# Kernel optimization log

Measured on AMD Instinct MI355X. Metric: run time of the kernel, lower is better.

The kernel has to match this reference:

```python
import jax, jax.numpy as jnp
import numpy as np

H, HK, D, WIN = 16, 4, 128, 1024  # n_head, n_kv_head, head_dim, left window


def rmsnorm(x):
    eps = jnp.asarray(jnp.finfo(x.dtype).eps, x.dtype)
    return x * jax.lax.rsqrt(jnp.mean(x * x, axis=-1, keepdims=True) + eps)


def rope(x, cos, sin):
    d = x.shape[-1] // 2
    x1, x2 = x[..., :d], x[..., d:]
    return jnp.concatenate([x1 * cos + x2 * sin, x1 * -sin + x2 * cos], axis=-1)


def setup_inputs() -> dict:
    key = jax.random.key(0)
    ks = jax.random.split(key, 12)
    B, T, C = 4, 2048, 2048
    t = jnp.arange(T, dtype=jnp.float32)[:, None]
    inv = 1.0 / (10000.0 ** (jnp.arange(D // 2, dtype=jnp.float32) / (D // 2)))
    ang = t * inv[None, :]  # [T, D/2]
    return {
        "x": jax.random.normal(ks[0], (B, T, C), jnp.float32),
        "x0": jax.random.normal(ks[1], (B, T, C), jnp.float32),
        "ve": jnp.zeros((B, T, C), jnp.float32),  # unused in add_init_qkv branch
        "cos": jnp.cos(ang)[None, :, None, :],  # [1,T,1,D/2]
        "sin": jnp.sin(ang)[None, :, None, :],
        "Wq": jax.random.normal(ks[2], (H * D, C), jnp.float32) * 0.02,
        "Wk": jax.random.normal(ks[3], (HK * D, C), jnp.float32) * 0.02,
        "Wv": jax.random.normal(ks[4], (HK * D, C), jnp.float32) * 0.02,
        "Wproj": jax.random.normal(ks[5], (C, H * D), jnp.float32) * 0.02,
        "alpha_q": jnp.ones((1,), jnp.float32),
        "beta_q": jax.random.uniform(ks[6], (1,), jnp.float32),
        "alpha_k": jnp.ones((1,), jnp.float32),
        "beta_k": jax.random.uniform(ks[7], (1,), jnp.float32),
        "alpha_v": jnp.ones((1,), jnp.float32),
        "beta_v": jax.random.uniform(ks[8], (1,), jnp.float32),
    }


def reference(x, x0, ve, cos, sin, Wq, Wk, Wv, Wproj,
              alpha_q, beta_q, alpha_k, beta_k, alpha_v, beta_v):
    B, T, C = x.shape
    g = H // HK  # GQA group size

    q = (x @ Wq.T).reshape(B, T, H, D)
    k = (x @ Wk.T).reshape(B, T, HK, D)
    v = (x @ Wv.T).reshape(B, T, HK, D)
    v_init = v

    # is_target + add_init_qkv + learn_init_coeffs: blend with projections of norm(x0)
    x0n = rmsnorm(x0)
    cqx = (x0n @ Wq.T).reshape(B, T, H, D)
    ckx = (x0n @ Wk.T).reshape(B, T, HK, D)
    cvx = (x0n @ Wv.T).reshape(B, T, HK, D)
    q = alpha_q * q + beta_q * cqx
    k = alpha_k * k + beta_k * ckx
    v = alpha_v * v + beta_v * cvx

    # rotary + qk-norm + 1.2 scale
    q = rmsnorm(rope(q, cos, sin)) * 1.2
    k = rmsnorm(rope(k, cos, sin)) * 1.2

    qg = q.reshape(B, T, HK, g, D)
    scale = 1.0 / np.sqrt(D)
    scores = jnp.einsum('bqhgd,bkhd->bhgqk', qg, k) * scale  # [B,HK,g,T,T]
    i = jnp.arange(T)[:, None]
    j = jnp.arange(T)[None, :]
    mask = (j <= i) & (i - j <= WIN)
    scores = jnp.where(mask, scores, -jnp.inf)
    p = jax.nn.softmax(scores, axis=-1)
    y = jnp.einsum('bhgqk,bkhd->bqhgd', p, v).reshape(B, T, H * D)

    y = y @ Wproj.T
    return (y, v_init)
```

## Files before the change

kernel.cpp:

```cpp
#include <hip/hip_runtime.h>
#include <hip/hip_bf16.h>
#include <math.h>


using bf16 = __hip_bfloat16;
typedef __attribute__((ext_vector_type(8))) short bf16x8;
typedef __attribute__((ext_vector_type(4))) short bf16x4;
typedef __attribute__((ext_vector_type(4))) float f32x4;

constexpr int Bb = 4, Ts = 2048, Cc = 2048, NH = 16, NKV = 4, Dh = 128, WIN = 1024;
constexpr float EPS = 1.1920929e-07f;

__device__ __forceinline__ void gld16(void* lds, const void* g) {
  __builtin_amdgcn_global_load_lds(
      (__attribute__((address_space(1))) unsigned int*)((void*)g),
      (__attribute__((address_space(3))) unsigned int*)lds, 16, 0, 0);
}

__device__ __forceinline__ unsigned short bfbits(float f) {
  bf16 h = __float2bfloat16(f);
  return __builtin_bit_cast(unsigned short, h);
}

__device__ __forceinline__ void store_out(float* p, float v) { *p = v; }
__device__ __forceinline__ void store_out(bf16* p, float v) { *p = __float2bfloat16(v); }

__device__ __forceinline__ f32x4 mfma16(bf16x4 a, bf16x4 b, f32x4 c) {
#if __has_builtin(__builtin_amdgcn_mfma_f32_16x16x16bf16_1k)
  return __builtin_amdgcn_mfma_f32_16x16x16bf16_1k(a, b, c, 0, 0, 0);
#else
  bf16x8 a8 = {a[0], a[1], a[2], a[3], 0, 0, 0, 0};
  bf16x8 b8 = {b[0], b[1], b[2], b[3], 0, 0, 0, 0};
  return __builtin_amdgcn_mfma_f32_16x16x32_bf16(a8, b8, c, 0, 0, 0);
#endif
}

__global__ __launch_bounds__(256) void convert_w(const float* __restrict__ src,
                                                 bf16* __restrict__ dst, int n4) {
  int i = blockIdx.x * 256 + threadIdx.x;
  if (i < n4) {
    float4 v = ((const float4*)src)[i];
    ushort4 u;
    u.x = bfbits(v.x); u.y = bfbits(v.y); u.z = bfbits(v.z); u.w = bfbits(v.w);
    ((ushort4*)dst)[i] = u;
  }
}

__global__ __launch_bounds__(256) void prep(
    const float* __restrict__ x, const float* __restrict__ x0,
    const float* aq_p, const float* bq_p, const float* ak_p, const float* bk_p,
    bf16* __restrict__ xq, bf16* __restrict__ xk,
    bf16* __restrict__ xb, bf16* __restrict__ x0n) {
  const int row = blockIdx.x, tid = threadIdx.x;
  const float4* xr = (const float4*)(x + (size_t)row * Cc);
  const float4* nr = (const float4*)(x0 + (size_t)row * Cc);
  float4 xa[2], na[2];
  float ss = 0.f;
#pragma unroll
  for (int j = 0; j < 2; ++j) {
    xa[j] = xr[tid + j * 256];
    na[j] = nr[tid + j * 256];
    ss += na[j].x * na[j].x + na[j].y * na[j].y + na[j].z * na[j].z + na[j].w * na[j].w;
  }
#pragma unroll
  for (int o = 32; o; o >>= 1) ss += __shfl_xor(ss, o);
  __shared__ float red[4];
  if ((tid & 63) == 0) red[tid >> 6] = ss;
  __syncthreads();
  const float rms = rsqrtf((red[0] + red[1] + red[2] + red[3]) * (1.f / Cc) + EPS);
  const float aq = *aq_p, bq = *bq_p, ak = *ak_p, bk = *bk_p;
#pragma unroll
  for (int j = 0; j < 2; ++j) {
    const size_t base = (size_t)row * Cc + (size_t)(tid + j * 256) * 4;
    float nx[4] = {na[j].x * rms, na[j].y * rms, na[j].z * rms, na[j].w * rms};
    float xv[4] = {xa[j].x, xa[j].y, xa[j].z, xa[j].w};
    ushort4 uq, uk, ub, un;
    uq.x = bfbits(aq * xv[0] + bq * nx[0]); uq.y = bfbits(aq * xv[1] + bq * nx[1]);
    uq.z = bfbits(aq * xv[2] + bq * nx[2]); uq.w = bfbits(aq * xv[3] + bq * nx[3]);
    uk.x = bfbits(ak * xv[0] + bk * nx[0]); uk.y = bfbits(ak * xv[1] + bk * nx[1]);
    uk.z = bfbits(ak * xv[2] + bk * nx[2]); uk.w = bfbits(ak * xv[3] + bk * nx[3]);
    ub.x = bfbits(xv[0]); ub.y = bfbits(xv[1]); ub.z = bfbits(xv[2]); ub.w = bfbits(xv[3]);
    un.x = bfbits(nx[0]); un.y = bfbits(nx[1]); un.z = bfbits(nx[2]); un.w = bfbits(nx[3]);
    *(ushort4*)(xq + base) = uq;
    *(ushort4*)(xk + base) = uk;
    *(ushort4*)(xb + base) = ub;
    *(ushort4*)(x0n + base) = un;
  }
}

template <typename OutT>
__device__ __forceinline__ void gemm_body(
    const bf16* __restrict__ A, const bf16* __restrict__ W,
    OutT* __restrict__ C, int N, int K) {
  __shared__ unsigned short sA[128 * 64];
  __shared__ unsigned short sB[128 * 64];
  const int tid = threadIdx.x, wave = tid >> 6, lane = tid & 63;
  const int quad = lane >> 4, l15 = lane & 15;
  const int bm = blockIdx.x * 128, bn = blockIdx.y * 128;
  const int wm = (wave >> 1) * 64, wn = (wave & 1) * 64;
  const int srow = wave * 32 + (lane >> 3);
  const int scol = (lane & 7) * 8;

  f32x4 acc[4][4] = {};

  for (int k0 = 0; k0 < K; k0 += 64) {
#pragma unroll
    for (int i = 0; i < 4; ++i) {
      gld16(&sA[(wave * 32 + i * 8) * 64], &A[(size_t)(bm + srow + i * 8) * K + k0 + scol]);
      gld16(&sB[(wave * 32 + i * 8) * 64], &W[(size_t)(bn + srow + i * 8) * K + k0 + scol]);
    }
    __syncthreads();
#pragma unroll
    for (int kk = 0; kk < 2; ++kk) {
      bf16x8 af[4], bfr[4];
#pragma unroll
      for (int t = 0; t < 4; ++t)
        af[t] = *(const bf16x8*)&sA[(wm + t * 16 + l15) * 64 + kk * 32 + quad * 8];
#pragma unroll
      for (int t = 0; t < 4; ++t)
        bfr[t] = *(const bf16x8*)&sB[(wn + t * 16 + l15) * 64 + kk * 32 + quad * 8];
#pragma unroll
      for (int tm = 0; tm < 4; ++tm)
#pragma unroll
        for (int tn = 0; tn < 4; ++tn)
          acc[tm][tn] = __builtin_amdgcn_mfma_f32_16x16x32_bf16(af[tm], bfr[tn], acc[tm][tn], 0, 0, 0);
    }
    __syncthreads();
  }
#pragma unroll
  for (int tm = 0; tm < 4; ++tm)
#pragma unroll
    for (int tn = 0; tn < 4; ++tn)
#pragma unroll
      for (int r = 0; r < 4; ++r) {
        const int row = bm + wm + tm * 16 + quad * 4 + r;
        const int col = bn + wn + tn * 16 + l15;
        store_out(&C[(size_t)row * N + col], acc[tm][tn][r]);
      }
}

template <typename OutT>
__global__ __launch_bounds__(256) void gemm_bt(
    const bf16* __restrict__ A, const bf16* __restrict__ W,
    OutT* __restrict__ C, int N, int K) {
  gemm_body<OutT>(A, W, C, N, K);
}

struct GemmTriple { const bf16* A; const bf16* W; bf16* C; };
struct GemmTriple3 { GemmTriple t[3]; };

__global__ __launch_bounds__(256) void gemm_bt3(GemmTriple3 g, int N, int K) {
  const GemmTriple tr = g.t[blockIdx.z];
  gemm_body<bf16>(tr.A, tr.W, tr.C, N, K);
}

__global__ __launch_bounds__(256) void post_qk(
    const bf16* __restrict__ pre, const float* __restrict__ cosp,
    const float* __restrict__ sinp, bf16* __restrict__ outh, int nh, float mult) {
  const int wid = blockIdx.x * 4 + (threadIdx.x >> 6);
  const int lane = threadIdx.x & 63;
  const int h = wid % nh;
  const int bt = wid / nh;
  const int t = bt & (Ts - 1);
  const int b = bt >> 11;
  const size_t src = (size_t)bt * (size_t)(nh * Dh) + (size_t)h * Dh;
  float x1 = __bfloat162float(pre[src + lane]);
  float x2 = __bfloat162float(pre[src + 64 + lane]);
  float c = cosp[t * 64 + lane], s = sinp[t * 64 + lane];
  float o1 = x1 * c + x2 * s;
  float o2 = x2 * c - x1 * s;
  float ss = o1 * o1 + o2 * o2;
#pragma unroll
  for (int o = 32; o; o >>= 1) ss += __shfl_xor(ss, o);
  const float r = rsqrtf(ss * (1.f / Dh) + EPS) * mult;
  const size_t dst = ((size_t)(b * nh + h) * Ts + t) * Dh;
  outh[dst + lane] = __float2bfloat16(o1 * r);
  outh[dst + 64 + lane] = __float2bfloat16(o2 * r);
}

__global__ __launch_bounds__(256) void post_v(
    const bf16* __restrict__ vinit, const bf16* __restrict__ cvx,
    const float* av_p, const float* bv_p,
    bf16* __restrict__ vth, float* __restrict__ vout) {
  __shared__ unsigned short vt[128 * 65];
  const int t0 = blockIdx.x * 64;
  const int b = blockIdx.y >> 2, hk = blockIdx.y & 3;
  const float av = *av_p, bv = *bv_p;
  const int tid = threadIdx.x;
  for (int j = 0; j < 32; ++j) {
    const int e = j * 256 + tid;
    const int tl = e >> 7, d = e & 127;
    const size_t src = (size_t)(b * Ts + t0 + tl) * (NKV * Dh) + hk * Dh + d;
    const float vi = __bfloat162float(vinit[src]);
    const float cv = __bfloat162float(cvx[src]);
    vout[src] = vi;
    vt[d * 65 + tl] = bfbits(av * vi + bv * cv);
  }
  __syncthreads();
#pragma unroll
  for (int j = 0; j < 4; ++j) {
    const int g = j * 256 + tid;
    const int d = g >> 3, t8 = (g & 7) * 8;
    const unsigned short* p = &vt[d * 65 + t8];
    uint4 u;
    u.x = p[0] | ((unsigned int)p[1] << 16);
    u.y = p[2] | ((unsigned int)p[3] << 16);
    u.z = p[4] | ((unsigned int)p[5] << 16);
    u.w = p[6] | ((unsigned int)p[7] << 16);
    *(uint4*)&vth[((size_t)(b * NKV + hk) * Dh + d) * Ts + t0 + t8] = u;
  }
}

__global__ __launch_bounds__(256) void attn(
    const bf16* __restrict__ qh, const bf16* __restrict__ kh,
    const bf16* __restrict__ vth, bf16* __restrict__ att) {
  __shared__ unsigned short sK[64 * 128];
  __shared__ unsigned short sV[128 * 64];

  const int tid = threadIdx.x, wave = tid >> 6, lane = tid & 63;
  const int quad = lane >> 4, l15 = lane & 15;
  const int q0 = blockIdx.x * 128;
  const int b = blockIdx.y >> 4, h = blockIdx.y & 15, hk = h >> 2;

  const bf16* Qp = qh + (size_t)(b * NH + h) * Ts * Dh;
  const bf16* Kp = kh + (size_t)(b * NKV + hk) * Ts * Dh;
  const bf16* Vp = vth + (size_t)(b * NKV + hk) * Dh * Ts;

  const int qw = q0 + wave * 32;

  bf16x8 qf[2][4];
#pragma unroll
  for (int tm = 0; tm < 2; ++tm)
#pragma unroll
    for (int kk = 0; kk < 4; ++kk)
      qf[tm][kk] = *(const bf16x8*)&Qp[(size_t)(qw + tm * 16 + l15) * Dh + kk * 32 + quad * 8];

  f32x4 of[2][8] = {};
  float m_i[2] = {-__builtin_inff(), -__builtin_inff()};
  float l_i[2] = {0.f, 0.f};

  const int krow = lane >> 4, kgp = lane & 15;
  const int vrow = lane >> 3, vgp = lane & 7;

  const int jt_lo = q0 >= WIN ? (q0 - WIN) >> 6 : 0;
  const int jt_hi = (q0 + 127) >> 6;

  for (int jt = jt_lo; jt <= jt_hi; ++jt) {
    const int j0 = jt << 6;
    __syncthreads();
#pragma unroll
    for (int i = 0; i < 4; ++i) {
      const int row = wave * 16 + i * 4 + krow;
      gld16(&sK[(wave * 16 + i * 4) * 128],
            &Kp[(size_t)(j0 + row) * Dh + (kgp ^ (row & 15)) * 8]);
      const int d = wave * 32 + i * 8 + vrow;
      gld16(&sV[(wave * 32 + i * 8) * 64],
            &Vp[(size_t)d * Ts + j0 + (vgp ^ (d & 7)) * 8]);
    }
    __syncthreads();

    if (j0 > qw + 31 || qw > j0 + 63 + WIN) continue;

    f32x4 sfT[4][2];
#pragma unroll
    for (int tn = 0; tn < 4; ++tn) {
      bf16x8 kf[4];
#pragma unroll
      for (int kk = 0; kk < 4; ++kk)
        kf[kk] = *(const bf16x8*)&sK[(tn * 16 + l15) * 128 + (((kk * 4 + quad) ^ l15) * 8)];
#pragma unroll
      for (int tm = 0; tm < 2; ++tm) {
        f32x4 a = {};
#pragma unroll
        for (int kk = 0; kk < 4; ++kk)
          a = __builtin_amdgcn_mfma_f32_16x16x32_bf16(kf[kk], qf[tm][kk], a, 0, 0, 0);
        sfT[tn][tm] = a;
      }
    }

    float alpha[2];
    bf16x4 pf[2][4];
#pragma unroll
    for (int tm = 0; tm < 2; ++tm) {
      const int dq = (qw + tm * 16 + l15) - (j0 + quad * 4);
      float mloc = -__builtin_inff();
#pragma unroll
      for (int tn = 0; tn < 4; ++tn)
#pragma unroll
        for (int r = 0; r < 4; ++r) {
          const unsigned diff = (unsigned)(dq - tn * 16 - r);
          float s = (diff <= (unsigned)WIN) ? sfT[tn][tm][r] : -__builtin_inff();
          sfT[tn][tm][r] = s;
          mloc = fmaxf(mloc, s);
        }
      mloc = fmaxf(mloc, __shfl_xor(mloc, 16));
      mloc = fmaxf(mloc, __shfl_xor(mloc, 32));
      const float mnew = fmaxf(m_i[tm], mloc);
      alpha[tm] = __builtin_amdgcn_exp2f(m_i[tm] - mnew);
      m_i[tm] = mnew;
      float rs = 0.f;
#pragma unroll
      for (int tn = 0; tn < 4; ++tn) {
        bf16x4 p4;
#pragma unroll
        for (int r = 0; r < 4; ++r) {
          const float p = __builtin_amdgcn_exp2f(sfT[tn][tm][r] - mnew);
          rs += p;
          p4[r] = (short)bfbits(p);
        }
        pf[tm][tn] = p4;
      }
      rs += __shfl_xor(rs, 16);
      rs += __shfl_xor(rs, 32);
      l_i[tm] = l_i[tm] * alpha[tm] + rs;
    }

#pragma unroll
    for (int tm = 0; tm < 2; ++tm) {
      float ar[4];
#pragma unroll
      for (int r = 0; r < 4; ++r) ar[r] = __shfl(alpha[tm], quad * 4 + r);
#pragma unroll
      for (int dn = 0; dn < 8; ++dn)
#pragma unroll
        for (int r = 0; r < 4; ++r) of[tm][dn][r] *= ar[r];
    }

#pragma unroll
    for (int tn = 0; tn < 4; ++tn) {
      const int gsw = (tn * 2) ^ (l15 & 7);
#pragma unroll
      for (int dn = 0; dn < 8; ++dn) {
        const int d = dn * 16 + l15;
        const bf16x4 vf = *(const bf16x4*)&sV[d * 64 + ((gsw ^ (quad >> 1)) * 8) + (quad & 1) * 4];
        of[0][dn] = mfma16(pf[0][tn], vf, of[0][dn]);
        of[1][dn] = mfma16(pf[1][tn], vf, of[1][dn]);
      }
    }
  }

#pragma unroll
  for (int tm = 0; tm < 2; ++tm) {
#pragma unroll
    for (int r = 0; r < 4; ++r) {
      const float lr = __shfl(l_i[tm], quad * 4 + r);
      const float inv = 1.f / lr;
      const int qr = qw + tm * 16 + quad * 4 + r;
      bf16* dst = att + (size_t)(b * Ts + qr) * (NH * Dh) + h * Dh;
#pragma unroll
      for (int dn = 0; dn < 8; ++dn)
        dst[dn * 16 + l15] = __float2bfloat16(of[tm][dn][r] * inv);
    }
  }
}

extern "C" void kernel_launch(void* const* d_in, const int* in_sizes, int n_in,
                              void* d_out, int out_size, void* d_ws, size_t ws_size,
                              hipStream_t stream) {
  const float* x = (const float*)d_in[0];
  const float* x0 = (const float*)d_in[1];
  const float* cosp = (const float*)d_in[3];
  const float* sinp = (const float*)d_in[4];
  const float* Wq = (const float*)d_in[5];
  const float* Wk = (const float*)d_in[6];
  const float* Wv = (const float*)d_in[7];
  const float* Wp = (const float*)d_in[8];
  const float* aq = (const float*)d_in[9];
  const float* bq = (const float*)d_in[10];
  const float* ak = (const float*)d_in[11];
  const float* bk = (const float*)d_in[12];
  const float* av = (const float*)d_in[13];
  const float* bv = (const float*)d_in[14];

  char* ws = (char*)d_ws;
  const size_t MB = 1024ull * 1024;
  bf16* xq = (bf16*)(ws + 0 * MB);
  bf16* xk = (bf16*)(ws + 32 * MB);
  bf16* xb = (bf16*)(ws + 64 * MB);
  bf16* x0n = (bf16*)(ws + 96 * MB);
  bf16* vinit = (bf16*)(ws + 128 * MB);
  bf16* cvx = (bf16*)(ws + 136 * MB);
  bf16* Wqb = (bf16*)(ws + 144 * MB);
  bf16* Wkb = (bf16*)(ws + 152 * MB);
  bf16* Wvb = (bf16*)(ws + 154 * MB);
  bf16* Wpb = (bf16*)(ws + 156 * MB);
  bf16* att = xq;
  bf16* qh = xk;
  bf16* kh = xb;
  bf16* vth = (bf16*)(ws + 72 * MB);

  float* y = (float*)d_out;
  float* vout = (float*)d_out + (size_t)Bb * Ts * Cc;
  bf16* q_pre = (bf16*)d_out;
  bf16* k_pre = (bf16*)vout;

  convert_w<<<4096, 256, 0, stream>>>(Wq, Wqb, 1048576);
  convert_w<<<1024, 256, 0, stream>>>(Wk, Wkb, 262144);
  convert_w<<<1024, 256, 0, stream>>>(Wv, Wvb, 262144);
  convert_w<<<4096, 256, 0, stream>>>(Wp, Wpb, 1048576);

  prep<<<8192, 256, 0, stream>>>(x, x0, aq, bq, ak, bk, xq, xk, xb, x0n);

  gemm_bt<bf16><<<dim3(64, 16), 256, 0, stream>>>(xq, Wqb, q_pre, 2048, 2048);

  GemmTriple3 g3;
  g3.t[0] = {xk, Wkb, k_pre};
  g3.t[1] = {xb, Wvb, vinit};
  g3.t[2] = {x0n, Wvb, cvx};
  gemm_bt3<<<dim3(64, 4, 3), 256, 0, stream>>>(g3, 512, 2048);

  const float qmult = 1.2f * 0.08838834764831845f * 1.4426950408889634f;
  post_qk<<<32768, 256, 0, stream>>>(q_pre, cosp, sinp, qh, NH, qmult);
  post_qk<<<8192, 256, 0, stream>>>(k_pre, cosp, sinp, kh, NKV, 1.2f);
  post_v<<<dim3(32, 16), 256, 0, stream>>>(vinit, cvx, av, bv, vth, vout);

  attn<<<dim3(16, 64), 256, 0, stream>>>(qh, kh, vth, att);

  gemm_bt<float><<<dim3(64, 16), 256, 0, stream>>>(att, Wpb, y, 2048, 2048);
}
```

Baseline: 790.5 us.

## Merge small launches, pre-blend V input, skip interior masking and rescale

Combines the four weight conversions into one kernel and the Q/K rope-norm passes into one launch. It also blends x and normalized x0 with the V coefficients in prep, so the V GEMM writes blended V directly and v_init is written as fp32 straight to the output, removing the post_v pass. In attention, interior tiles skip mask evaluation and the output rescale is skipped when the running max is unchanged. This trades a few extra branches for fewer launches and less intermediate memory traffic.

```diff
diff --git a/kernel.cpp b/kernel.cpp
--- a/kernel.cpp
+++ b/kernel.cpp
@@ -35,22 +35,30 @@
 #endif
 }
 
-__global__ __launch_bounds__(256) void convert_w(const float* __restrict__ src,
-                                                 bf16* __restrict__ dst, int n4) {
+__global__ __launch_bounds__(256) void convert_all(
+    const float* __restrict__ s0, const float* __restrict__ s1,
+    const float* __restrict__ s2, const float* __restrict__ s3,
+    bf16* __restrict__ d0, bf16* __restrict__ d1,
+    bf16* __restrict__ d2, bf16* __restrict__ d3) {
   int i = blockIdx.x * 256 + threadIdx.x;
-  if (i < n4) {
-    float4 v = ((const float4*)src)[i];
-    ushort4 u;
-    u.x = bfbits(v.x); u.y = bfbits(v.y); u.z = bfbits(v.z); u.w = bfbits(v.w);
-    ((ushort4*)dst)[i] = u;
-  }
+  const float* s;
+  bf16* d;
+  if (i < 1048576) { s = s0; d = d0; }
+  else if (i < 1310720) { s = s1; d = d1; i -= 1048576; }
+  else if (i < 1572864) { s = s2; d = d2; i -= 1310720; }
+  else { s = s3; d = d3; i -= 1572864; }
+  float4 v = ((const float4*)s)[i];
+  ushort4 u;
+  u.x = bfbits(v.x); u.y = bfbits(v.y); u.z = bfbits(v.z); u.w = bfbits(v.w);
+  ((ushort4*)d)[i] = u;
 }
 
 __global__ __launch_bounds__(256) void prep(
     const float* __restrict__ x, const float* __restrict__ x0,
     const float* aq_p, const float* bq_p, const float* ak_p, const float* bk_p,
+    const float* av_p, const float* bv_p,
     bf16* __restrict__ xq, bf16* __restrict__ xk,
-    bf16* __restrict__ xb, bf16* __restrict__ x0n) {
+    bf16* __restrict__ xb, bf16* __restrict__ xvm) {
   const int row = blockIdx.x, tid = threadIdx.x;
   const float4* xr = (const float4*)(x + (size_t)row * Cc);
   const float4* nr = (const float4*)(x0 + (size_t)row * Cc);
@@ -68,23 +76,24 @@
   if ((tid & 63) == 0) red[tid >> 6] = ss;
   __syncthreads();
   const float rms = rsqrtf((red[0] + red[1] + red[2] + red[3]) * (1.f / Cc) + EPS);
-  const float aq = *aq_p, bq = *bq_p, ak = *ak_p, bk = *bk_p;
+  const float aq = *aq_p, bq = *bq_p, ak = *ak_p, bk = *bk_p, av = *av_p, bv = *bv_p;
 #pragma unroll
   for (int j = 0; j < 2; ++j) {
     const size_t base = (size_t)row * Cc + (size_t)(tid + j * 256) * 4;
     float nx[4] = {na[j].x * rms, na[j].y * rms, na[j].z * rms, na[j].w * rms};
     float xv[4] = {xa[j].x, xa[j].y, xa[j].z, xa[j].w};
-    ushort4 uq, uk, ub, un;
+    ushort4 uq, uk, ub, uv;
     uq.x = bfbits(aq * xv[0] + bq * nx[0]); uq.y = bfbits(aq * xv[1] + bq * nx[1]);
     uq.z = bfbits(aq * xv[2] + bq * nx[2]); uq.w = bfbits(aq * xv[3] + bq * nx[3]);
     uk.x = bfbits(ak * xv[0] + bk * nx[0]); uk.y = bfbits(ak * xv[1] + bk * nx[1]);
     uk.z = bfbits(ak * xv[2] + bk * nx[2]); uk.w = bfbits(ak * xv[3] + bk * nx[3]);
     ub.x = bfbits(xv[0]); ub.y = bfbits(xv[1]); ub.z = bfbits(xv[2]); ub.w = bfbits(xv[3]);
-    un.x = bfbits(nx[0]); un.y = bfbits(nx[1]); un.z = bfbits(nx[2]); un.w = bfbits(nx[3]);
+    uv.x = bfbits(av * xv[0] + bv * nx[0]); uv.y = bfbits(av * xv[1] + bv * nx[1]);
+    uv.z = bfbits(av * xv[2] + bv * nx[2]); uv.w = bfbits(av * xv[3] + bv * nx[3]);
     *(ushort4*)(xq + base) = uq;
     *(ushort4*)(xk + base) = uk;
     *(ushort4*)(xb + base) = ub;
-    *(ushort4*)(x0n + base) = un;
+    *(ushort4*)(xvm + base) = uv;
   }
 }
 
@@ -146,21 +155,31 @@
   gemm_body<OutT>(A, W, C, N, K);
 }
 
-struct GemmTriple { const bf16* A; const bf16* W; bf16* C; };
-struct GemmTriple3 { GemmTriple t[3]; };
-
-__global__ __launch_bounds__(256) void gemm_bt3(GemmTriple3 g, int N, int K) {
-  const GemmTriple tr = g.t[blockIdx.z];
-  gemm_body<bf16>(tr.A, tr.W, tr.C, N, K);
-}
-
-__global__ __launch_bounds__(256) void post_qk(
-    const bf16* __restrict__ pre, const float* __restrict__ cosp,
-    const float* __restrict__ sinp, bf16* __restrict__ outh, int nh, float mult) {
+struct GT { const bf16* A; const bf16* W; void* C; int isf32; };
+struct GT3 { GT t[3]; };
+
+__global__ __launch_bounds__(256) void gemm_bt3(GT3 g, int N, int K) {
+  const GT tr = g.t[blockIdx.z];
+  if (tr.isf32)
+    gemm_body<float>(tr.A, tr.W, (float*)tr.C, N, K);
+  else
+    gemm_body<bf16>(tr.A, tr.W, (bf16*)tr.C, N, K);
+}
+
+__global__ __launch_bounds__(256) void post_qk2(
+    const bf16* __restrict__ qpre, const bf16* __restrict__ kpre,
+    const float* __restrict__ cosp, const float* __restrict__ sinp,
+    bf16* __restrict__ qh, bf16* __restrict__ kh, float qmult, float kmult) {
   const int wid = blockIdx.x * 4 + (threadIdx.x >> 6);
   const int lane = threadIdx.x & 63;
-  const int h = wid % nh;
-  const int bt = wid / nh;
+  const bf16* pre;
+  bf16* outh;
+  int nh, idx;
+  float mult;
+  if (wid < Bb * Ts * NH) { pre = qpre; outh = qh; nh = NH; idx = wid; mult = qmult; }
+  else { pre = kpre; outh = kh; nh = NKV; idx = wid - Bb * Ts * NH; mult = kmult; }
+  const int h = idx % nh;
+  const int bt = idx / nh;
   const int t = bt & (Ts - 1);
   const int b = bt >> 11;
   const size_t src = (size_t)bt * (size_t)(nh * Dh) + (size_t)h * Dh;
@@ -178,23 +197,17 @@
   outh[dst + 64 + lane] = __float2bfloat16(o2 * r);
 }
 
-__global__ __launch_bounds__(256) void post_v(
-    const bf16* __restrict__ vinit, const bf16* __restrict__ cvx,
-    const float* av_p, const float* bv_p,
-    bf16* __restrict__ vth, float* __restrict__ vout) {
+__global__ __launch_bounds__(256) void transpose_v(
+    const unsigned short* __restrict__ vtmp, bf16* __restrict__ vth) {
   __shared__ unsigned short vt[128 * 65];
   const int t0 = blockIdx.x * 64;
   const int b = blockIdx.y >> 2, hk = blockIdx.y & 3;
-  const float av = *av_p, bv = *bv_p;
   const int tid = threadIdx.x;
+#pragma unroll
   for (int j = 0; j < 32; ++j) {
     const int e = j * 256 + tid;
     const int tl = e >> 7, d = e & 127;
-    const size_t src = (size_t)(b * Ts + t0 + tl) * (NKV * Dh) + hk * Dh + d;
-    const float vi = __bfloat162float(vinit[src]);
-    const float cv = __bfloat162float(cvx[src]);
-    vout[src] = vi;
-    vt[d * 65 + tl] = bfbits(av * vi + bv * cv);
+    vt[d * 65 + tl] = vtmp[(size_t)(b * Ts + t0 + tl) * (NKV * Dh) + hk * Dh + d];
   }
   __syncthreads();
 #pragma unroll
@@ -278,33 +291,47 @@
       }
     }
 
+    const bool interior = (j0 + 63 <= qw) && (qw + 31 - j0 <= WIN);
+
     float alpha[2];
+    bool upd[2];
     bf16x4 pf[2][4];
 #pragma unroll
     for (int tm = 0; tm < 2; ++tm) {
-      const int dq = (qw + tm * 16 + l15) - (j0 + quad * 4);
       float mloc = -__builtin_inff();
-#pragma unroll
-      for (int tn = 0; tn < 4; ++tn)
-#pragma unroll
-        for (int r = 0; r < 4; ++r) {
-          const unsigned diff = (unsigned)(dq - tn * 16 - r);
-          float s = (diff <= (unsigned)WIN) ? sfT[tn][tm][r] : -__builtin_inff();
-          sfT[tn][tm][r] = s;
-          mloc = fmaxf(mloc, s);
-        }
+      if (interior) {
+#pragma unroll
+        for (int tn = 0; tn < 4; ++tn)
+#pragma unroll
+          for (int r = 0; r < 4; ++r) mloc = fmaxf(mloc, sfT[tn][tm][r]);
+      } else {
+        const int dq = (qw + tm * 16 + l15) - (j0 + quad * 4);
+#pragma unroll
+        for (int tn = 0; tn < 4; ++tn)
+#pragma unroll
+          for (int r = 0; r < 4; ++r) {
+            const unsigned diff = (unsigned)(dq - tn * 16 - r);
+            float s = (diff <= (unsigned)WIN) ? sfT[tn][tm][r] : -__builtin_inff();
+            sfT[tn][tm][r] = s;
+            mloc = fmaxf(mloc, s);
+          }
+      }
       mloc = fmaxf(mloc, __shfl_xor(mloc, 16));
       mloc = fmaxf(mloc, __shfl_xor(mloc, 32));
-      const float mnew = fmaxf(m_i[tm], mloc);
-      alpha[tm] = __builtin_amdgcn_exp2f(m_i[tm] - mnew);
-      m_i[tm] = mnew;
+      upd[tm] = __any(mloc > m_i[tm]);
+      alpha[tm] = 1.f;
+      if (upd[tm]) {
+        const float mnew = fmaxf(m_i[tm], mloc);
+        alpha[tm] = __builtin_amdgcn_exp2f(m_i[tm] - mnew);
+        m_i[tm] = mnew;
+      }
       float rs = 0.f;
 #pragma unroll
       for (int tn = 0; tn < 4; ++tn) {
         bf16x4 p4;
 #pragma unroll
         for (int r = 0; r < 4; ++r) {
-          const float p = __builtin_amdgcn_exp2f(sfT[tn][tm][r] - mnew);
+          const float p = __builtin_amdgcn_exp2f(sfT[tn][tm][r] - m_i[tm]);
           rs += p;
           p4[r] = (short)bfbits(p);
         }
@@ -317,13 +344,15 @@
 
 #pragma unroll
     for (int tm = 0; tm < 2; ++tm) {
-      float ar[4];
-#pragma unroll
-      for (int r = 0; r < 4; ++r) ar[r] = __shfl(alpha[tm], quad * 4 + r);
-#pragma unroll
-      for (int dn = 0; dn < 8; ++dn)
-#pragma unroll
-        for (int r = 0; r < 4; ++r) of[tm][dn][r] *= ar[r];
+      if (upd[tm]) {
+        float ar[4];
+#pragma unroll
+        for (int r = 0; r < 4; ++r) ar[r] = __shfl(alpha[tm], quad * 4 + r);
+#pragma unroll
+        for (int dn = 0; dn < 8; ++dn)
+#pragma unroll
+          for (int r = 0; r < 4; ++r) of[tm][dn][r] *= ar[r];
+      }
     }
 
 #pragma unroll
@@ -377,9 +406,9 @@
   bf16* xq = (bf16*)(ws + 0 * MB);
   bf16* xk = (bf16*)(ws + 32 * MB);
   bf16* xb = (bf16*)(ws + 64 * MB);
-  bf16* x0n = (bf16*)(ws + 96 * MB);
-  bf16* vinit = (bf16*)(ws + 128 * MB);
-  bf16* cvx = (bf16*)(ws + 136 * MB);
+  bf16* xvm = (bf16*)(ws + 96 * MB);
+  bf16* k_pre = (bf16*)(ws + 128 * MB);
+  bf16* vtmp = (bf16*)(ws + 136 * MB);
   bf16* Wqb = (bf16*)(ws + 144 * MB);
   bf16* Wkb = (bf16*)(ws + 152 * MB);
   bf16* Wvb = (bf16*)(ws + 154 * MB);
@@ -392,27 +421,23 @@
   float* y = (float*)d_out;
   float* vout = (float*)d_out + (size_t)Bb * Ts * Cc;
   bf16* q_pre = (bf16*)d_out;
-  bf16* k_pre = (bf16*)vout;
-
-  convert_w<<<4096, 256, 0, stream>>>(Wq, Wqb, 1048576);
-  convert_w<<<1024, 256, 0, stream>>>(Wk, Wkb, 262144);
-  convert_w<<<1024, 256, 0, stream>>>(Wv, Wvb, 262144);
-  convert_w<<<4096, 256, 0, stream>>>(Wp, Wpb, 1048576);
-
-  prep<<<8192, 256, 0, stream>>>(x, x0, aq, bq, ak, bk, xq, xk, xb, x0n);
+
+  convert_all<<<10240, 256, 0, stream>>>(Wq, Wk, Wv, Wp, Wqb, Wkb, Wvb, Wpb);
+
+  prep<<<8192, 256, 0, stream>>>(x, x0, aq, bq, ak, bk, av, bv, xq, xk, xb, xvm);
 
   gemm_bt<bf16><<<dim3(64, 16), 256, 0, stream>>>(xq, Wqb, q_pre, 2048, 2048);
 
-  GemmTriple3 g3;
-  g3.t[0] = {xk, Wkb, k_pre};
-  g3.t[1] = {xb, Wvb, vinit};
-  g3.t[2] = {x0n, Wvb, cvx};
+  GT3 g3;
+  g3.t[0] = {xk, Wkb, (void*)k_pre, 0};
+  g3.t[1] = {xb, Wvb, (void*)vout, 1};
+  g3.t[2] = {xvm, Wvb, (void*)vtmp, 0};
   gemm_bt3<<<dim3(64, 4, 3), 256, 0, stream>>>(g3, 512, 2048);
 
   const float qmult = 1.2f * 0.08838834764831845f * 1.4426950408889634f;
-  post_qk<<<32768, 256, 0, stream>>>(q_pre, cosp, sinp, qh, NH, qmult);
-  post_qk<<<8192, 256, 0, stream>>>(k_pre, cosp, sinp, kh, NKV, 1.2f);
-  post_v<<<dim3(32, 16), 256, 0, stream>>>(vinit, cvx, av, bv, vth, vout);
+  post_qk2<<<40960, 256, 0, stream>>>(q_pre, k_pre, cosp, sinp, qh, kh, qmult, 1.2f);
+
+  transpose_v<<<dim3(32, 16), 256, 0, stream>>>((const unsigned short*)vtmp, vth);
 
   attn<<<dim3(16, 64), 256, 0, stream>>>(qh, kh, vth, att);
 
```

Result: slower. 822.2 us (+4.0%).
